# Performance work log

Measured on AMD Instinct MI355X. Metric: run time of the kernel, lower is better.

## Reference

```python
import jax, jax.numpy as jnp
import numpy as np

D_MODEL = 2048
NQ = 16      # query heads
NKV = 4      # kv heads (GQA)
DH = 128     # content head dim
DR = 64      # rope head dim
DKV = 512    # kv latent dim
DQC = 1536   # q latent dim
B, S = 2, 2048
DT = DH + DR


def rotate_half(x):
    x1, x2 = jnp.split(x, 2, axis=-1)
    return jnp.concatenate([-x2, x1], axis=-1)


def setup_inputs() -> dict:
    key = jax.random.key(0)
    ks = jax.random.split(key, 10)
    sc = 0.02
    x = jax.random.normal(ks[0], (B, S, D_MODEL), jnp.float32)
    positions = jnp.arange(S, dtype=jnp.int32)
    # standard RoPE cache over the rope subspace
    inv_freq = 1.0 / (10000.0 ** (jnp.arange(0, DR, 2, dtype=jnp.float32) / DR))
    ang = positions.astype(jnp.float32)[:, None] * inv_freq[None, :]   # [S, DR/2]
    emb = jnp.concatenate([ang, ang], axis=-1)                         # [S, DR]
    cos_cache = jnp.cos(emb)
    sin_cache = jnp.sin(emb)
    attn_mask = jnp.tril(jnp.ones((S, S), dtype=bool))                 # causal, True=attend
    # weights stored [in, out] (torch Linear weight transposed)
    W_DKV = sc * jax.random.normal(ks[1], (D_MODEL, DKV), jnp.float32)
    W_UK = sc * jax.random.normal(ks[2], (DKV, NKV * DH), jnp.float32)
    W_UV = sc * jax.random.normal(ks[3], (DKV, NKV * DH), jnp.float32)
    W_DQ = sc * jax.random.normal(ks[4], (D_MODEL, DQC), jnp.float32)
    W_UQ = sc * jax.random.normal(ks[5], (DQC, NQ * DH), jnp.float32)
    W_KR = sc * jax.random.normal(ks[6], (D_MODEL, NKV * DR), jnp.float32)
    W_QR = sc * jax.random.normal(ks[7], (D_MODEL, NQ * DR), jnp.float32)
    W_O = sc * jax.random.normal(ks[8], (NQ * DH, D_MODEL), jnp.float32)
    return {"x": x, "cos_cache": cos_cache, "sin_cache": sin_cache,
            "positions": positions, "attn_mask": attn_mask,
            "W_DKV": W_DKV, "W_UK": W_UK, "W_UV": W_UV, "W_DQ": W_DQ,
            "W_UQ": W_UQ, "W_KR": W_KR, "W_QR": W_QR, "W_O": W_O}


def reference(x, cos_cache, sin_cache, positions, attn_mask,
              W_DKV, W_UK, W_UV, W_DQ, W_UQ, W_KR, W_QR, W_O):
    b, s, _ = x.shape
    cos = cos_cache[positions][None, None]  # [1,1,S,DR]
    sin = sin_cache[positions][None, None]
    # low-rank KV latent (this is the MLA cache)
    c_kv = x @ W_DKV                                                 # [B,S,DKV]
    K_rope = (x @ W_KR).reshape(b, s, NKV, DR).transpose(0, 2, 1, 3)  # [B,NKV,S,DR]
    K_rope = K_rope * cos + rotate_half(K_rope) * sin
    # decompress K/V content from latent
    K_content = (c_kv @ W_UK).reshape(b, s, NKV, DH).transpose(0, 2, 1, 3)  # [B,NKV,S,DH]
    V = (c_kv @ W_UV).reshape(b, s, NKV, DH).transpose(0, 2, 1, 3)          # [B,NKV,S,DH]
    # queries via low-rank path + rope subspace
    c_q = x @ W_DQ
    Q_content = (c_q @ W_UQ).reshape(b, s, NQ, DH).transpose(0, 2, 1, 3)    # [B,NQ,S,DH]
    Q_rope = (x @ W_QR).reshape(b, s, NQ, DR).transpose(0, 2, 1, 3)         # [B,NQ,S,DR]
    Q_rope = Q_rope * cos + rotate_half(Q_rope) * sin
    Q = jnp.concatenate([Q_content, Q_rope], axis=-1)   # [B,NQ,S,DT]
    K = jnp.concatenate([K_content, K_rope], axis=-1)   # [B,NKV,S,DT]
    # GQA: group query heads over shared kv heads (no materialized repeat)
    G = NQ // NKV
    Qg = Q.reshape(b, NKV, G, s, DT)
    scores = jnp.einsum('bkgsd,bktd->bkgst', Qg, K) / np.float32(np.sqrt(DT))
    scores = jnp.where(attn_mask[None, None, None], scores, -jnp.inf)
    w = jax.nn.softmax(scores, axis=-1)
    attn = jnp.einsum('bkgst,bktd->bkgsd', w, V)         # [B,NKV,G,S,DH]
    attn = attn.reshape(b, NQ, s, DH).transpose(0, 2, 1, 3).reshape(b, s, NQ * DH)
    out = attn @ W_O                                     # [B,S,D_MODEL]
    return out, c_kv, K_rope
```

## Files before the change

kernel.cpp:

```cpp
#include <hip/hip_runtime.h>
#include <stdint.h>

typedef unsigned short u16;
typedef unsigned int u32;

#define B_    2
#define S_    2048
#define NQ_   16
#define NKV_  4
#define DH_   128
#define DR_   64
#define DT_   192
#define M_    4096

using short8 = __attribute__((ext_vector_type(8))) short;
using f32x4  = __attribute__((ext_vector_type(4))) float;
using half8  = __attribute__((ext_vector_type(8))) _Float16;
using u16x4  = __attribute__((ext_vector_type(4))) u16;

__device__ __forceinline__ float cl(float f) {
    return fminf(fmaxf(f, -3.38e38f), 3.38e38f);
}
__device__ __forceinline__ u16 f2b(float f) {
    union { float f; u32 u; } v; v.f = f;
    u32 u = v.u;
    return (u16)((u + 0x7fffu + ((u >> 16) & 1u)) >> 16);
}
__device__ __forceinline__ void gload16(const void* g, void* l) {
    __builtin_amdgcn_global_load_lds(
        (const __attribute__((address_space(1))) void*)g,
        (__attribute__((address_space(3))) void*)l,
        16, 0, 0);
}

__global__ __launch_bounds__(256) void x_f16(const float* __restrict__ X,
                                             _Float16* __restrict__ F) {
    size_t i = ((size_t)blockIdx.x * 256 + threadIdx.x) * 8;
    float4 a = *(const float4*)(X + i);
    float4 b4 = *(const float4*)(X + i + 4);
    float va[8] = {a.x, a.y, a.z, a.w, b4.x, b4.y, b4.z, b4.w};
    half8 f;
#pragma unroll
    for (int j = 0; j < 8; ++j) f[j] = (_Float16)va[j];
    *(half8*)(F + i) = f;
}

__global__ __launch_bounds__(256) void wt_f16(const float* __restrict__ W,
                                              _Float16* __restrict__ T,
                                              int K, int N) {
    __shared__ float tile[32][33];
    int k0 = blockIdx.x * 32, n0 = blockIdx.y * 32;
    int tx = threadIdx.x, ty = threadIdx.y;
#pragma unroll
    for (int i = 0; i < 32; i += 8)
        tile[ty + i][tx] = W[(size_t)(k0 + ty + i) * N + n0 + tx];
    __syncthreads();
#pragma unroll
    for (int i = 0; i < 32; i += 8)
        T[(size_t)(n0 + ty + i) * K + k0 + tx] = (_Float16)tile[tx][ty + i];
}

__global__ __launch_bounds__(256) void gemm_f16(const _Float16* __restrict__ A, int lda,
                                                const _Float16* __restrict__ Bt,
                                                void* __restrict__ p0,
                                                void* __restrict__ p1,
                                                void* __restrict__ p2,
                                                float cscale, int mode,
                                                int N, int K) {
    __shared__ __align__(16) _Float16 lA[128 * 32];
    __shared__ __align__(16) _Float16 lB[128 * 32];
    const int t = threadIdx.x, lane = t & 63, w = t >> 6;
    const int quad = lane >> 4, l16 = lane & 15;
    const int wr = w >> 1, wc = w & 1;
    const int m0 = blockIdx.y * 128, n0 = blockIdx.x * 128;
    f32x4 acc[4][4] = {};

    for (int kt = 0; kt < K; kt += 32) {
        __syncthreads();
#pragma unroll
        for (int c = 0; c < 2; ++c) {
            const int chunk = c * 256 + t;
            const int row = chunk >> 2, co = (chunk & 3) * 8;
            const int lofs = (c * 256 + w * 64) * 8;
            gload16(A + (size_t)(m0 + row) * lda + kt + co, lA + lofs);
            gload16(Bt + (size_t)(n0 + row) * K + kt + co, lB + lofs);
        }
        __syncthreads();
        half8 af[4], bf4[4];
#pragma unroll
        for (int i = 0; i < 4; ++i) {
            af[i]  = *(const half8*)&lA[(wr * 64 + i * 16 + l16) * 32 + quad * 8];
            bf4[i] = *(const half8*)&lB[(wc * 64 + i * 16 + l16) * 32 + quad * 8];
        }
#pragma unroll
        for (int i = 0; i < 4; ++i)
#pragma unroll
            for (int j = 0; j < 4; ++j)
                acc[i][j] = __builtin_amdgcn_mfma_f32_16x16x32_f16(af[i], bf4[j], acc[i][j], 0, 0, 0);
    }
#pragma unroll
    for (int i = 0; i < 4; ++i)
#pragma unroll
        for (int j = 0; j < 4; ++j) {
            const int mbase = m0 + wr * 64 + i * 16 + quad * 4;
            const int nn = n0 + wc * 64 + j * 16 + l16;
            if (mode == 0) {
                float* C = (float*)p0;
#pragma unroll
                for (int r = 0; r < 4; ++r)
                    C[(size_t)(mbase + r) * N + nn] = cl(acc[i][j][r]);
            } else if (mode == 1) {
                _Float16* Cf = (_Float16*)p0;
#pragma unroll
                for (int r = 0; r < 4; ++r)
                    Cf[(size_t)(mbase + r) * N + nn] = (_Float16)acc[i][j][r];
            } else if (mode == 2) {
                u16* Q = (u16*)p0;
                const int h = nn >> 7, dcol = nn & 127;
#pragma unroll
                for (int r = 0; r < 4; ++r)
                    Q[(size_t)(mbase + r) * 3072 + h * 192 + dcol] =
                        f2b(acc[i][j][r] * cscale);
            } else if (mode == 3) {
                const int bb = mbase >> 11, s = mbase & 2047;
                if (nn < 512) {
                    u16* Kp = (u16*)p0;
                    const int kv = nn >> 7, d = nn & 127;
                    const size_t rb = ((size_t)((bb * 4 + kv) * 2048 + s)) * 192 + d;
#pragma unroll
                    for (int r = 0; r < 4; ++r)
                        Kp[rb + (size_t)r * 192] = f2b(acc[i][j][r]);
                } else {
                    u16* Vt = (u16*)p1;
                    const int e = nn - 512, kv = e >> 7, d = e & 127;
                    u16x4 pk;
                    pk[0] = f2b(acc[i][j][0]); pk[1] = f2b(acc[i][j][1]);
                    pk[2] = f2b(acc[i][j][2]); pk[3] = f2b(acc[i][j][3]);
                    *(u16x4*)&((u16*)Vt)[((size_t)((bb * 4 + kv) * 128 + d)) * 2048 + s] = pk;
                }
            } else {
                if (nn < 512) {
                    float* ckv = (float*)p0;
                    _Float16* ckf = (_Float16*)p1;
#pragma unroll
                    for (int r = 0; r < 4; ++r) {
                        float v = acc[i][j][r];
                        ckv[(size_t)(mbase + r) * 512 + nn] = cl(v);
                        ckf[(size_t)(mbase + r) * 512 + nn] = (_Float16)v;
                    }
                } else {
                    float* krr = (float*)p2;
#pragma unroll
                    for (int r = 0; r < 4; ++r)
                        krr[(size_t)(mbase + r) * 256 + (nn - 512)] = acc[i][j][r];
                }
            }
        }
}

__global__ __launch_bounds__(256) void rope_q16(const _Float16* __restrict__ dqr,
                                                const float* __restrict__ cosc,
                                                const float* __restrict__ sinc,
                                                const int* __restrict__ pos,
                                                u16* __restrict__ qb16) {
    const float sc = 0.07216878364870322f;
    int t = blockIdx.x * 256 + threadIdx.x;
    int d = t & 31, h = (t >> 5) & 15, rowi = t >> 9;
    int s = rowi & 2047;
    int p = pos[s];
    float c1 = cosc[p * 64 + d],      s1 = sinc[p * 64 + d];
    float c2 = cosc[p * 64 + 32 + d], s2 = sinc[p * 64 + 32 + d];
    const _Float16* base = dqr + (size_t)rowi * 2560 + 1536 + h * 64;
    float x1 = (float)base[d];
    float x2 = (float)base[d + 32];
    u16* q = qb16 + (size_t)rowi * 3072 + h * 192 + 128;
    q[d]      = f2b((x1 * c1 - x2 * s1) * sc);
    q[d + 32] = f2b((x2 * c2 + x1 * s2) * sc);
}

__global__ __launch_bounds__(256) void rope_k(const float* __restrict__ krr,
                                              const float* __restrict__ cosc,
                                              const float* __restrict__ sinc,
                                              const int* __restrict__ pos,
                                              float* __restrict__ Krope,
                                              u16* __restrict__ Kp) {
    int t = blockIdx.x * 256 + threadIdx.x;
    int d = t & 31, kv = (t >> 5) & 3, rowi = t >> 7;
    int b = rowi >> 11, s = rowi & 2047;
    int p = pos[s];
    float c1 = cosc[p * 64 + d],      s1 = sinc[p * 64 + d];
    float c2 = cosc[p * 64 + 32 + d], s2 = sinc[p * 64 + 32 + d];
    float x1 = krr[(size_t)rowi * 256 + kv * 64 + d];
    float x2 = krr[(size_t)rowi * 256 + kv * 64 + 32 + d];
    float o1 = x1 * c1 - x2 * s1;
    float o2 = x2 * c2 + x1 * s2;
    int g = b * NKV_ + kv;
    size_t ob = ((size_t)(g * S_) + s) * 64;
    Krope[ob + d]      = cl(o1);
    Krope[ob + 32 + d] = cl(o2);
    u16* kp = Kp + ((size_t)(g * S_ + s)) * 192 + 128;
    kp[d]      = f2b(o1);
    kp[32 + d] = f2b(o2);
}

__global__ __launch_bounds__(256) void attn_mfma(const u16* __restrict__ qb16,
                                                 const u16* __restrict__ Kp,
                                                 const u16* __restrict__ Vt,
                                                 _Float16* __restrict__ atf) {
    __shared__ __align__(16) u16 lK[64 * 200];
    __shared__ __align__(16) u16 lVt[144 * 72];
    __shared__ __align__(16) u16 lP[4][16 * 72];

    const int t = threadIdx.x, lane = t & 63, w = t >> 6;
    const int quad = lane >> 4, l16 = lane & 15;
    const int id = blockIdx.x;
    const int g = id & 7;
    const int b = g >> 2;
    const int k = id >> 3;
    const int h = (g & 3) * 4 + (k & 3);
    const int px = k >> 2;

#pragma unroll
    for (int c = 0; c < 4; ++c) {
        int i = c * 256 + t;
        int rr = 128 + (i >> 6), ccol = i & 63;
        lVt[rr * 72 + ccol] = (rr == 128) ? (u16)0x3F80 : (u16)0;
    }

    for (int ph = 0; ph < 2; ++ph) {
        const int qt = ph ? px : (31 - px);
        const int q0 = qt * 64;
        const int iw = q0 + w * 16;

        short8 qf[6];
        {
            const u16* qp = qb16 + ((size_t)(b * S_ + iw + l16)) * 3072 + h * 192;
#pragma unroll
            for (int kc = 0; kc < 6; ++kc)
                qf[kc] = *(const short8*)&qp[kc * 32 + quad * 8];
        }

        f32x4 O9[9] = {};
        float mr[4] = {-1e30f, -1e30f, -1e30f, -1e30f};

        const int ntile = qt + 1;
        for (int tile = 0; tile < ntile; ++tile) {
            const int j0 = tile * 64;
            __syncthreads();
#pragma unroll
            for (int c = 0; c < 6; ++c) {
                int seg = c * 256 + t;
                int row = seg / 24, ch = (seg % 24) * 8;
                *(uint4*)&lK[row * 200 + ch] =
                    *(const uint4*)&Kp[((size_t)g * S_ + j0 + row) * 192 + ch];
            }
#pragma unroll
            for (int c = 0; c < 4; ++c) {
                int seg = c * 256 + t;
                int d = seg >> 3, ch = (seg & 7) * 8;
                *(uint4*)&lVt[d * 72 + ch] =
                    *(const uint4*)&Vt[((size_t)g * 128 + d) * S_ + j0 + ch];
            }
            __syncthreads();

            f32x4 s4[4];
            __builtin_amdgcn_s_setprio(1);
#pragma unroll
            for (int cc = 0; cc < 4; ++cc) {
                f32x4 sx = {};
#pragma unroll
                for (int kc = 0; kc < 6; ++kc) {
                    short8 kf = *(const short8*)&lK[(cc * 16 + l16) * 200 + kc * 32 + quad * 8];
                    sx = __builtin_amdgcn_mfma_f32_16x16x32_bf16(qf[kc], kf, sx, 0, 0, 0);
                }
                s4[cc] = sx;
            }
            __builtin_amdgcn_s_setprio(0);

            float sv[4][4];
#pragma unroll
            for (int cc = 0; cc < 4; ++cc)
#pragma unroll
                for (int r = 0; r < 4; ++r) {
                    int ir = iw + quad * 4 + r;
                    sv[cc][r] = (j0 + cc * 16 + l16 <= ir) ? s4[cc][r] : -1e30f;
                }
            float tm[4];
#pragma unroll
            for (int r = 0; r < 4; ++r)
                tm[r] = fmaxf(fmaxf(sv[0][r], sv[1][r]), fmaxf(sv[2][r], sv[3][r]));
#pragma unroll
            for (int m = 1; m < 16; m <<= 1)
#pragma unroll
                for (int r = 0; r < 4; ++r) tm[r] = fmaxf(tm[r], __shfl_xor(tm[r], m));
            int small = (tm[0] <= mr[0] + 8.f) && (tm[1] <= mr[1] + 8.f) &&
                        (tm[2] <= mr[2] + 8.f) && (tm[3] <= mr[3] + 8.f);
            if (!__all(small)) {
                float al[4];
#pragma unroll
                for (int r = 0; r < 4; ++r) {
                    float mn = fmaxf(mr[r], tm[r]);
                    al[r] = __expf(mr[r] - mn);
                    mr[r] = mn;
                }
#pragma unroll
                for (int dc = 0; dc < 9; ++dc)
#pragma unroll
                    for (int r = 0; r < 4; ++r) O9[dc][r] *= al[r];
            }
            float p[4][4];
#pragma unroll
            for (int cc = 0; cc < 4; ++cc)
#pragma unroll
                for (int r = 0; r < 4; ++r)
                    p[cc][r] = __expf(sv[cc][r] - mr[r]);
#pragma unroll
            for (int cc = 0; cc < 4; ++cc)
#pragma unroll
                for (int r = 0; r < 4; ++r)
                    lP[w][(quad * 4 + r) * 72 + cc * 16 + l16] = f2b(p[cc][r]);
            short8 pf0 = *(const short8*)&lP[w][l16 * 72 + quad * 8];
            short8 pf1 = *(const short8*)&lP[w][l16 * 72 + 32 + quad * 8];
            __builtin_amdgcn_s_setprio(1);
#pragma unroll
            for (int dc = 0; dc < 9; ++dc) {
                short8 vf0 = *(const short8*)&lVt[(dc * 16 + l16) * 72 + quad * 8];
                short8 vf1 = *(const short8*)&lVt[(dc * 16 + l16) * 72 + 32 + quad * 8];
                O9[dc] = __builtin_amdgcn_mfma_f32_16x16x32_bf16(pf0, vf0, O9[dc], 0, 0, 0);
                O9[dc] = __builtin_amdgcn_mfma_f32_16x16x32_bf16(pf1, vf1, O9[dc], 0, 0, 0);
            }
            __builtin_amdgcn_s_setprio(0);
        }
        float inv[4];
#pragma unroll
        for (int r = 0; r < 4; ++r) {
            float lr = __shfl(O9[8][r], quad * 16);
            inv[r] = 1.f / fmaxf(lr, 1e-30f);
        }
#pragma unroll
        for (int dc = 0; dc < 8; ++dc)
#pragma unroll
            for (int r = 0; r < 4; ++r) {
                int ir = iw + quad * 4 + r;
                atf[((size_t)(b * S_ + ir)) * 2048 + h * 128 + dc * 16 + l16] =
                    (_Float16)cl(O9[dc][r] * inv[r]);
            }
    }
}

extern "C" void kernel_launch(void* const* d_in, const int* in_sizes, int n_in,
                              void* d_out, int out_size, void* d_ws, size_t ws_size,
                              hipStream_t stream) {
    const float* x     = (const float*)d_in[0];
    const float* cosc  = (const float*)d_in[1];
    const float* sinc  = (const float*)d_in[2];
    const int*   pos   = (const int*)d_in[3];
    const float* W_DKV = (const float*)d_in[5];
    const float* W_UK  = (const float*)d_in[6];
    const float* W_UV  = (const float*)d_in[7];
    const float* W_DQ  = (const float*)d_in[8];
    const float* W_UQ  = (const float*)d_in[9];
    const float* W_KR  = (const float*)d_in[10];
    const float* W_QR  = (const float*)d_in[11];
    const float* W_O   = (const float*)d_in[12];
    (void)ws_size;

    float* outp      = (float*)d_out;
    float* ckv_out   = outp + 8388608;
    float* krope_out = outp + 10485760;

    char* w = (char*)d_ws;
    auto alloc = [&](size_t bytes) { char* p = w; w += bytes; return p; };
    _Float16* xf   = (_Float16*)alloc(16777216);
    _Float16* ckf  = (_Float16*)alloc(4194304);
    float*    krr  = (float*)alloc(4194304);
    _Float16* dqr  = (_Float16*)alloc(20971520);
    u16*      qb16 = (u16*)alloc(25165824);
    u16*      Kp   = (u16*)alloc(6291456);
    u16*      Vt   = (u16*)alloc(4194304);
    _Float16* atf  = (_Float16*)alloc(16777216);
    _Float16* Wdkr = (_Float16*)alloc(3145728);
    _Float16* Wdqr = (_Float16*)alloc(10485760);
    _Float16* Wuq  = (_Float16*)alloc(6291456);
    _Float16* Wukv = (_Float16*)alloc(1048576);
    _Float16* Wo   = (_Float16*)alloc(8388608);

    const float sc = 0.07216878364870322f;
    const dim3 tb(32, 8);

    x_f16<<<4096, 256, 0, stream>>>(x, xf);
    wt_f16<<<dim3(64, 16), tb, 0, stream>>>(W_DKV, Wdkr, 2048, 512);
    wt_f16<<<dim3(64, 8),  tb, 0, stream>>>(W_KR,  Wdkr + (size_t)512 * 2048, 2048, 256);
    wt_f16<<<dim3(64, 48), tb, 0, stream>>>(W_DQ,  Wdqr, 2048, 1536);
    wt_f16<<<dim3(64, 32), tb, 0, stream>>>(W_QR,  Wdqr + (size_t)1536 * 2048, 2048, 1024);
    wt_f16<<<dim3(48, 64), tb, 0, stream>>>(W_UQ,  Wuq, 1536, 2048);
    wt_f16<<<dim3(16, 16), tb, 0, stream>>>(W_UK,  Wukv, 512, 512);
    wt_f16<<<dim3(16, 16), tb, 0, stream>>>(W_UV,  Wukv + (size_t)512 * 512, 512, 512);
    wt_f16<<<dim3(64, 64), tb, 0, stream>>>(W_O,   Wo, 2048, 2048);

    gemm_f16<<<dim3(6, 32), 256, 0, stream>>>(xf, 2048, Wdkr,
                                              ckv_out, ckf, krr, 1.f, 4, 768, 2048);
    gemm_f16<<<dim3(20, 32), 256, 0, stream>>>(xf, 2048, Wdqr,
                                               dqr, nullptr, nullptr, 1.f, 1, 2560, 2048);
    gemm_f16<<<dim3(16, 32), 256, 0, stream>>>(dqr, 2560, Wuq,
                                               qb16, nullptr, nullptr, sc, 2, 2048, 1536);
    gemm_f16<<<dim3(8, 32), 256, 0, stream>>>(ckf, 512, Wukv,
                                              Kp, Vt, nullptr, 1.f, 3, 1024, 512);

    rope_q16<<<8192, 256, 0, stream>>>(dqr, cosc, sinc, pos, qb16);
    rope_k<<<2048, 256, 0, stream>>>(krr, cosc, sinc, pos, krope_out, Kp);

    attn_mfma<<<512, 256, 0, stream>>>(qb16, Kp, Vt, atf);
    gemm_f16<<<dim3(16, 32), 256, 0, stream>>>(atf, 2048, Wo,
                                               outp, nullptr, nullptr, 1.f, 0, 2048, 2048);
}
```

Baseline: 526.4 us.

## Merge projection GEMMs, register-prefetch K/V tiles, and skip masking on interior tiles

```diff
diff --git a/kernel.cpp b/kernel.cpp
--- a/kernel.cpp
+++ b/kernel.cpp
@@ -60,19 +60,17 @@
         T[(size_t)(n0 + ty + i) * K + k0 + tx] = (_Float16)tile[tx][ty + i];
 }
 
-__global__ __launch_bounds__(256) void gemm_f16(const _Float16* __restrict__ A, int lda,
-                                                const _Float16* __restrict__ Bt,
-                                                void* __restrict__ p0,
-                                                void* __restrict__ p1,
-                                                void* __restrict__ p2,
-                                                float cscale, int mode,
-                                                int N, int K) {
-    __shared__ __align__(16) _Float16 lA[128 * 32];
-    __shared__ __align__(16) _Float16 lB[128 * 32];
+__device__ __forceinline__ void gemm_body(const _Float16* __restrict__ A, int lda,
+                                          const _Float16* __restrict__ Bt,
+                                          void* p0, void* p1, void* p2,
+                                          void* p3, void* p4,
+                                          float cscale, int mode,
+                                          int N, int K, int bx,
+                                          _Float16* lA, _Float16* lB) {
     const int t = threadIdx.x, lane = t & 63, w = t >> 6;
     const int quad = lane >> 4, l16 = lane & 15;
     const int wr = w >> 1, wc = w & 1;
-    const int m0 = blockIdx.y * 128, n0 = blockIdx.x * 128;
+    const int m0 = blockIdx.y * 128, n0 = bx * 128;
     f32x4 acc[4][4] = {};
 
     for (int kt = 0; kt < K; kt += 32) {
@@ -109,11 +107,6 @@
 #pragma unroll
                 for (int r = 0; r < 4; ++r)
                     C[(size_t)(mbase + r) * N + nn] = cl(acc[i][j][r]);
-            } else if (mode == 1) {
-                _Float16* Cf = (_Float16*)p0;
-#pragma unroll
-                for (int r = 0; r < 4; ++r)
-                    Cf[(size_t)(mbase + r) * N + nn] = (_Float16)acc[i][j][r];
             } else if (mode == 2) {
                 u16* Q = (u16*)p0;
                 const int h = nn >> 7, dcol = nn & 127;
@@ -148,17 +141,56 @@
                         ckv[(size_t)(mbase + r) * 512 + nn] = cl(v);
                         ckf[(size_t)(mbase + r) * 512 + nn] = (_Float16)v;
                     }
-                } else {
+                } else if (nn < 768) {
                     float* krr = (float*)p2;
 #pragma unroll
                     for (int r = 0; r < 4; ++r)
                         krr[(size_t)(mbase + r) * 256 + (nn - 512)] = acc[i][j][r];
+                } else if (nn < 2304) {
+                    _Float16* dqc = (_Float16*)p3;
+#pragma unroll
+                    for (int r = 0; r < 4; ++r)
+                        dqc[(size_t)(mbase + r) * 1536 + (nn - 768)] = (_Float16)acc[i][j][r];
+                } else {
+                    _Float16* qrf = (_Float16*)p4;
+#pragma unroll
+                    for (int r = 0; r < 4; ++r)
+                        qrf[(size_t)(mbase + r) * 1024 + (nn - 2304)] = (_Float16)acc[i][j][r];
                 }
             }
         }
 }
 
-__global__ __launch_bounds__(256) void rope_q16(const _Float16* __restrict__ dqr,
+__global__ __launch_bounds__(256) void gemm_f16(const _Float16* __restrict__ A, int lda,
+                                                const _Float16* __restrict__ Bt,
+                                                void* p0, void* p1, void* p2,
+                                                void* p3, void* p4,
+                                                float cscale, int mode,
+                                                int N, int K) {
+    __shared__ __align__(16) _Float16 lA[128 * 32];
+    __shared__ __align__(16) _Float16 lB[128 * 32];
+    gemm_body(A, lda, Bt, p0, p1, p2, p3, p4, cscale, mode, N, K, blockIdx.x, lA, lB);
+}
+
+__global__ __launch_bounds__(256) void gemm_uqkv(const _Float16* __restrict__ dqc,
+                                                 const _Float16* __restrict__ Wuq,
+                                                 u16* __restrict__ qb16, float sc,
+                                                 const _Float16* __restrict__ ckf,
+                                                 const _Float16* __restrict__ Wukv,
+                                                 u16* __restrict__ Kp,
+                                                 u16* __restrict__ Vt) {
+    __shared__ __align__(16) _Float16 lA[128 * 32];
+    __shared__ __align__(16) _Float16 lB[128 * 32];
+    const int bx = blockIdx.x;
+    if (bx < 16)
+        gemm_body(dqc, 1536, Wuq, qb16, nullptr, nullptr, nullptr, nullptr,
+                  sc, 2, 2048, 1536, bx, lA, lB);
+    else
+        gemm_body(ckf, 512, Wukv, Kp, Vt, nullptr, nullptr, nullptr,
+                  1.f, 3, 1024, 512, bx - 16, lA, lB);
+}
+
+__global__ __launch_bounds__(256) void rope_q16(const _Float16* __restrict__ qrf,
                                                 const float* __restrict__ cosc,
                                                 const float* __restrict__ sinc,
                                                 const int* __restrict__ pos,
@@ -170,7 +202,7 @@
     int p = pos[s];
     float c1 = cosc[p * 64 + d],      s1 = sinc[p * 64 + d];
     float c2 = cosc[p * 64 + 32 + d], s2 = sinc[p * 64 + 32 + d];
-    const _Float16* base = dqr + (size_t)rowi * 2560 + 1536 + h * 64;
+    const _Float16* base = qrf + (size_t)rowi * 1024 + h * 64;
     float x1 = (float)base[d];
     float x2 = (float)base[d + 32];
     u16* q = qb16 + (size_t)rowi * 3072 + h * 192 + 128;
@@ -227,6 +259,25 @@
         lVt[rr * 72 + ccol] = (rr == 128) ? (u16)0x3F80 : (u16)0;
     }
 
+    uint4 kreg0, kreg1, kreg2, kreg3, kreg4, kreg5;
+    uint4 vreg0, vreg1, vreg2, vreg3;
+#define PREFETCH(j0)                                                            \
+    {                                                                           \
+        const int _j0 = (j0);                                                   \
+        { int seg = t;            kreg0 = *(const uint4*)&Kp[((size_t)g * S_ + _j0 + seg / 24) * 192 + (seg % 24) * 8]; } \
+        { int seg = 256 + t;      kreg1 = *(const uint4*)&Kp[((size_t)g * S_ + _j0 + seg / 24) * 192 + (seg % 24) * 8]; } \
+        { int seg = 512 + t;      kreg2 = *(const uint4*)&Kp[((size_t)g * S_ + _j0 + seg / 24) * 192 + (seg % 24) * 8]; } \
+        { int seg = 768 + t;      kreg3 = *(const uint4*)&Kp[((size_t)g * S_ + _j0 + seg / 24) * 192 + (seg % 24) * 8]; } \
+        { int seg = 1024 + t;     kreg4 = *(const uint4*)&Kp[((size_t)g * S_ + _j0 + seg / 24) * 192 + (seg % 24) * 8]; } \
+        { int seg = 1280 + t;     kreg5 = *(const uint4*)&Kp[((size_t)g * S_ + _j0 + seg / 24) * 192 + (seg % 24) * 8]; } \
+        { int seg = t;            vreg0 = *(const uint4*)&Vt[((size_t)g * 128 + (seg >> 3)) * S_ + _j0 + (seg & 7) * 8]; } \
+        { int seg = 256 + t;      vreg1 = *(const uint4*)&Vt[((size_t)g * 128 + (seg >> 3)) * S_ + _j0 + (seg & 7) * 8]; } \
+        { int seg = 512 + t;      vreg2 = *(const uint4*)&Vt[((size_t)g * 128 + (seg >> 3)) * S_ + _j0 + (seg & 7) * 8]; } \
+        { int seg = 768 + t;      vreg3 = *(const uint4*)&Vt[((size_t)g * 128 + (seg >> 3)) * S_ + _j0 + (seg & 7) * 8]; } \
+    }
+
+    PREFETCH(0);
+
     for (int ph = 0; ph < 2; ++ph) {
         const int qt = ph ? px : (31 - px);
         const int q0 = qt * 64;
@@ -247,21 +298,19 @@
         for (int tile = 0; tile < ntile; ++tile) {
             const int j0 = tile * 64;
             __syncthreads();
-#pragma unroll
-            for (int c = 0; c < 6; ++c) {
-                int seg = c * 256 + t;
-                int row = seg / 24, ch = (seg % 24) * 8;
-                *(uint4*)&lK[row * 200 + ch] =
-                    *(const uint4*)&Kp[((size_t)g * S_ + j0 + row) * 192 + ch];
-            }
-#pragma unroll
-            for (int c = 0; c < 4; ++c) {
-                int seg = c * 256 + t;
-                int d = seg >> 3, ch = (seg & 7) * 8;
-                *(uint4*)&lVt[d * 72 + ch] =
-                    *(const uint4*)&Vt[((size_t)g * 128 + d) * S_ + j0 + ch];
-            }
+            { int seg = t;        *(uint4*)&lK[(seg / 24) * 200 + (seg % 24) * 8] = kreg0; }
+            { int seg = 256 + t;  *(uint4*)&lK[(seg / 24) * 200 + (seg % 24) * 8] = kreg1; }
+            { int seg = 512 + t;  *(uint4*)&lK[(seg / 24) * 200 + (seg % 24) * 8] = kreg2; }
+            { int seg = 768 + t;  *(uint4*)&lK[(seg / 24) * 200 + (seg % 24) * 8] = kreg3; }
+            { int seg = 1024 + t; *(uint4*)&lK[(seg / 24) * 200 + (seg % 24) * 8] = kreg4; }
+            { int seg = 1280 + t; *(uint4*)&lK[(seg / 24) * 200 + (seg % 24) * 8] = kreg5; }
+            { int seg = t;        *(uint4*)&lVt[(seg >> 3) * 72 + (seg & 7) * 8] = vreg0; }
+            { int seg = 256 + t;  *(uint4*)&lVt[(seg >> 3) * 72 + (seg & 7) * 8] = vreg1; }
+            { int seg = 512 + t;  *(uint4*)&lVt[(seg >> 3) * 72 + (seg & 7) * 8] = vreg2; }
+            { int seg = 768 + t;  *(uint4*)&lVt[(seg >> 3) * 72 + (seg & 7) * 8] = vreg3; }
             __syncthreads();
+            if (tile + 1 < ntile)      PREFETCH(j0 + 64)
+            else if (ph == 0)          PREFETCH(0)
 
             f32x4 s4[4];
             __builtin_amdgcn_s_setprio(1);
@@ -281,10 +330,16 @@
 #pragma unroll
             for (int cc = 0; cc < 4; ++cc)
 #pragma unroll
-                for (int r = 0; r < 4; ++r) {
-                    int ir = iw + quad * 4 + r;
-                    sv[cc][r] = (j0 + cc * 16 + l16 <= ir) ? s4[cc][r] : -1e30f;
-                }
+                for (int r = 0; r < 4; ++r) sv[cc][r] = s4[cc][r];
+            if (tile == ntile - 1) {
+#pragma unroll
+                for (int cc = 0; cc < 4; ++cc)
+#pragma unroll
+                    for (int r = 0; r < 4; ++r) {
+                        int ir = iw + quad * 4 + r;
+                        if (j0 + cc * 16 + l16 > ir) sv[cc][r] = -1e30f;
+                    }
+            }
             float tm[4];
 #pragma unroll
             for (int r = 0; r < 4; ++r)
@@ -346,6 +401,7 @@
                     (_Float16)cl(O9[dc][r] * inv[r]);
             }
     }
+#undef PREFETCH
 }
 
 extern "C" void kernel_launch(void* const* d_in, const int* in_sizes, int n_in,
@@ -374,13 +430,13 @@
     _Float16* xf   = (_Float16*)alloc(16777216);
     _Float16* ckf  = (_Float16*)alloc(4194304);
     float*    krr  = (float*)alloc(4194304);
-    _Float16* dqr  = (_Float16*)alloc(20971520);
+    _Float16* dqc  = (_Float16*)alloc(12582912);
+    _Float16* qrf  = (_Float16*)alloc(8388608);
     u16*      qb16 = (u16*)alloc(25165824);
     u16*      Kp   = (u16*)alloc(6291456);
     u16*      Vt   = (u16*)alloc(4194304);
     _Float16* atf  = (_Float16*)alloc(16777216);
-    _Float16* Wdkr = (_Float16*)alloc(3145728);
-    _Float16* Wdqr = (_Float16*)alloc(10485760);
+    _Float16* Wmeg = (_Float16*)alloc(13631488);
     _Float16* Wuq  = (_Float16*)alloc(6291456);
     _Float16* Wukv = (_Float16*)alloc(1048576);
     _Float16* Wo   = (_Float16*)alloc(8388608);
@@ -389,28 +445,26 @@
     const dim3 tb(32, 8);
 
     x_f16<<<4096, 256, 0, stream>>>(x, xf);
-    wt_f16<<<dim3(64, 16), tb, 0, stream>>>(W_DKV, Wdkr, 2048, 512);
-    wt_f16<<<dim3(64, 8),  tb, 0, stream>>>(W_KR,  Wdkr + (size_t)512 * 2048, 2048, 256);
-    wt_f16<<<dim3(64, 48), tb, 0, stream>>>(W_DQ,  Wdqr, 2048, 1536);
-    wt_f16<<<dim3(64, 32), tb, 0, stream>>>(W_QR,  Wdqr + (size_t)1536 * 2048, 2048, 1024);
+    wt_f16<<<dim3(64, 16), tb, 0, stream>>>(W_DKV, Wmeg, 2048, 512);
+    wt_f16<<<dim3(64, 8),  tb, 0, stream>>>(W_KR,  Wmeg + (size_t)512 * 2048, 2048, 256);
+    wt_f16<<<dim3(64, 48), tb, 0, stream>>>(W_DQ,  Wmeg + (size_t)768 * 2048, 2048, 1536);
+    wt_f16<<<dim3(64, 32), tb, 0, stream>>>(W_QR,  Wmeg + (size_t)2304 * 2048, 2048, 1024);
     wt_f16<<<dim3(48, 64), tb, 0, stream>>>(W_UQ,  Wuq, 1536, 2048);
     wt_f16<<<dim3(16, 16), tb, 0, stream>>>(W_UK,  Wukv, 512, 512);
     wt_f16<<<dim3(16, 16), tb, 0, stream>>>(W_UV,  Wukv + (size_t)512 * 512, 512, 512);
     wt_f16<<<dim3(64, 64), tb, 0, stream>>>(W_O,   Wo, 2048, 2048);
 
-    gemm_f16<<<dim3(6, 32), 256, 0, stream>>>(xf, 2048, Wdkr,
-                                              ckv_out, ckf, krr, 1.f, 4, 768, 2048);
-    gemm_f16<<<dim3(20, 32), 256, 0, stream>>>(xf, 2048, Wdqr,
-                                               dqr, nullptr, nullptr, 1.f, 1, 2560, 2048);
-    gemm_f16<<<dim3(16, 32), 256, 0, stream>>>(dqr, 2560, Wuq,
-                                               qb16, nullptr, nullptr, sc, 2, 2048, 1536);
-    gemm_f16<<<dim3(8, 32), 256, 0, stream>>>(ckf, 512, Wukv,
-                                              Kp, Vt, nullptr, 1.f, 3, 1024, 512);
-
-    rope_q16<<<8192, 256, 0, stream>>>(dqr, cosc, sinc, pos, qb16);
+    gemm_f16<<<dim3(26, 32), 256, 0, stream>>>(xf, 2048, Wmeg,
+                                               ckv_out, ckf, krr, dqc, qrf,
+                                               1.f, 6, 3328, 2048);
+    gemm_uqkv<<<dim3(24, 32), 256, 0, stream>>>(dqc, Wuq, qb16, sc,
+                                                ckf, Wukv, Kp, Vt);
+
+    rope_q16<<<8192, 256, 0, stream>>>(qrf, cosc, sinc, pos, qb16);
     rope_k<<<2048, 256, 0, stream>>>(krr, cosc, sinc, pos, krope_out, Kp);
 
     attn_mfma<<<512, 256, 0, stream>>>(qb16, Kp, Vt, atf);
     gemm_f16<<<dim3(16, 32), 256, 0, stream>>>(atf, 2048, Wo,
-                                               outp, nullptr, nullptr, 1.f, 0, 2048, 2048);
-}
+                                               outp, nullptr, nullptr, nullptr, nullptr,
+                                               1.f, 0, 2048, 2048);
+}
```

Result: slower. 559.9 us (+6.4%).
